# Kernel optimization log

Hardware: AMD Instinct MI355X
Metric: run time of the kernel (lower is better)

## Reference

```python
import jax, jax.numpy as jnp
import numpy as np

N_NODES = 50000
N_EDGES = 800000
HID = 64
NUM_CURR = 15
NUM_PAY = 7
CURR_DIM = 8
PAY_DIM = 4
NUM_NUM = 5
EDGE_REPR = 2 * HID + 2 * CURR_DIM + PAY_DIM + NUM_NUM  # 153


def setup_inputs() -> dict:
    key = jax.random.key(0)
    ks = jax.random.split(key, 24)
    f = lambda k, shape, scale=0.05: jax.random.normal(k, shape, jnp.float32) * scale
    inp = {
        'node_feats': jax.random.normal(ks[0], (N_NODES, 2), jnp.float32),
        'src': jax.random.randint(ks[1], (N_EDGES,), 0, N_NODES, jnp.int32),
        'dst': jax.random.randint(ks[2], (N_EDGES,), 0, N_NODES, jnp.int32),
        'payment_currency': jax.random.randint(ks[3], (N_EDGES,), 0, NUM_CURR, jnp.int32),
        'receiving_currency': jax.random.randint(ks[4], (N_EDGES,), 0, NUM_CURR, jnp.int32),
        'payment_format': jax.random.randint(ks[5], (N_EDGES,), 0, NUM_PAY, jnp.int32),
        'numericals': jax.random.normal(ks[6], (N_EDGES, NUM_NUM), jnp.float32),
        # GCN layer params
        'W0': f(ks[7], (2, HID)), 'b0': f(ks[8], (HID,)),
        'W1': f(ks[9], (HID, HID)), 'b1': f(ks[10], (HID,)),
        'W2': f(ks[11], (HID, HID)), 'b2': f(ks[12], (HID,)),
        # edge embeddings
        'curr_emb': f(ks[13], (NUM_CURR, CURR_DIM), 1.0),
        'pay_emb': f(ks[14], (NUM_PAY, PAY_DIM), 1.0),
        # edge classifier MLP
        'M0': f(ks[15], (EDGE_REPR, HID)), 'bM0': f(ks[16], (HID,)),
        'M1': f(ks[17], (HID, HID)), 'bM1': f(ks[18], (HID,)),
        'M2': f(ks[19], (HID, 2)), 'bM2': f(ks[20], (2,)),
    }
    return inp


def reference(node_feats, src, dst, payment_currency, receiving_currency,
              payment_format, numericals, W0, b0, W1, b1, W2, b2,
              curr_emb, pay_emb, M0, bM0, M1, bM1, M2, bM2):
    # symmetric-ish GCN norm: deg^{-1/2} on source (message) and dest (after sum)
    ones = jnp.ones((src.shape[0],), jnp.float32)
    deg = jax.ops.segment_sum(ones, dst, num_segments=N_NODES)
    norm = jnp.clip(deg, 1.0, None) ** -0.5  # [N]
    norm = norm[:, None]

    def gcn(h, W, b, residual):
        Wh = h @ W + b                         # [N, HID]
        m = Wh[src] * norm[src]                # gather-scale per edge [E, HID]
        agg = jax.ops.segment_sum(m, dst, num_segments=N_NODES)  # scatter-sum
        out = jax.nn.relu(agg * norm)
        return out + h if residual else out    # res_linear is Identity (dims match)

    h = gcn(node_feats, W0, b0, False)
    h = gcn(h, W1, b1, True)
    h = gcn(h, W2, b2, True)
    # dropout is inference no-op

    edge_repr = jnp.concatenate([
        h[src], h[dst],
        curr_emb[payment_currency], curr_emb[receiving_currency],
        pay_emb[payment_format], numericals,
    ], axis=1)  # [E, 153]

    x = jax.nn.relu(edge_repr @ M0 + bM0)
    x = jax.nn.relu(x @ M1 + bM1)
    logits = x @ M2 + bM2  # [E, 2]
    return logits
```

## Files before the change

kernel.cpp:

```cpp
#include <hip/hip_runtime.h>
#include <hip/hip_bf16.h>

#define N_NODES 50000
#define N_EDGES 800000
#define HID 64

__device__ __forceinline__ unsigned short f2bf(float f) {
    union { float f; unsigned int i; } v;
    v.f = f;
    unsigned int b = v.i;
    return (unsigned short)((b + 0x7FFFu + ((b >> 16) & 1u)) >> 16);
}

__device__ __forceinline__ void add_bf16_row(float* x, const unsigned short* row) {
    const uint4* r4 = (const uint4*)row;
#pragma unroll
    for (int q = 0; q < 8; ++q) {
        uint4 v = r4[q];
        union { unsigned int i; float f; } t;
        t.i = v.x << 16;         x[q*8 + 0] += t.f;
        t.i = v.x & 0xFFFF0000u; x[q*8 + 1] += t.f;
        t.i = v.y << 16;         x[q*8 + 2] += t.f;
        t.i = v.y & 0xFFFF0000u; x[q*8 + 3] += t.f;
        t.i = v.z << 16;         x[q*8 + 4] += t.f;
        t.i = v.z & 0xFFFF0000u; x[q*8 + 5] += t.f;
        t.i = v.w << 16;         x[q*8 + 6] += t.f;
        t.i = v.w & 0xFFFF0000u; x[q*8 + 7] += t.f;
    }
}


__global__ void k_deg(const int* __restrict__ dst, int* __restrict__ deg, int n) {
    int e = blockIdx.x * blockDim.x + threadIdx.x;
    if (e < n) atomicAdd(&deg[dst[e]], 1);
}

__global__ void k_off(const int* __restrict__ deg, int* __restrict__ row_ptr,
                      int* __restrict__ cursor, float* __restrict__ norm,
                      int* __restrict__ gcount, int n) {
    int i = blockIdx.x * blockDim.x + threadIdx.x;
    int lane = threadIdx.x & 63;
    int v = (i < n) ? deg[i] : 0;
    int s = v;
#pragma unroll
    for (int off = 1; off < 64; off <<= 1) {
        int t = __shfl_up(s, off);
        if (lane >= off) s += t;
    }
    int total = __shfl(s, 63);
    int base = 0;
    if (lane == 63) base = atomicAdd(gcount, total);
    base = __shfl(base, 63);
    int ex = base + s - v;
    if (i < n) {
        row_ptr[i] = ex;
        cursor[i]  = ex;
        norm[i] = 1.0f / sqrtf(fmaxf((float)v, 1.0f));
    }
}

__global__ void k_scatter(const int* __restrict__ src, const int* __restrict__ dst,
                          int* __restrict__ cursor, int* __restrict__ csr_src, int n) {
    int e = blockIdx.x * blockDim.x + threadIdx.x;
    if (e < n) {
        int d = dst[e];
        int pos = atomicAdd(&cursor[d], 1);
        csr_src[pos] = src[e];
    }
}


__global__ __launch_bounds__(256) void k_l0(const float2* __restrict__ nf,
                                            const float* __restrict__ norm,
                                            const int* __restrict__ row_ptr,
                                            const int* __restrict__ deg,
                                            const int* __restrict__ csr_src,
                                            const float* __restrict__ W0,
                                            const float* __restrict__ b0,
                                            float* __restrict__ h,
                                            float* __restrict__ hn,
                                            float* __restrict__ snorm, int n_nodes) {
    int lane = threadIdx.x & 63, wid = threadIdx.x >> 6;
    int n = blockIdx.x * 4 + wid;
    if (n >= n_nodes) return;
    int r0 = row_ptr[n], dc = deg[n];
    float a0 = 0.f, a1 = 0.f, sn = 0.f;
    for (int i = lane; i < dc; i += 64) {
        int s = csr_src[r0 + i];
        float ns = norm[s];
        float2 v = nf[s];
        a0 += v.x * ns;
        a1 += v.y * ns;
        sn += ns;
    }
#pragma unroll
    for (int off = 32; off; off >>= 1) {
        a0 += __shfl_xor(a0, off);
        a1 += __shfl_xor(a1, off);
        sn += __shfl_xor(sn, off);
    }
    float nn = norm[n];
    float v = (a0 * W0[lane] + a1 * W0[64 + lane] + b0[lane] * sn) * nn;
    v = fmaxf(v, 0.f);
    h[(size_t)n * 64 + lane] = v;
    hn[(size_t)n * 64 + lane] = v * nn;
    if (lane == 0) snorm[n] = sn;
}


__global__ __launch_bounds__(256) void k_agg(const float* __restrict__ hn,
                                             const int* __restrict__ row_ptr,
                                             const int* __restrict__ deg,
                                             const int* __restrict__ csr_src,
                                             float* __restrict__ g, int n_nodes) {
    int lane = threadIdx.x & 63, wid = threadIdx.x >> 6;
    int n = blockIdx.x * 4 + wid;
    if (n >= n_nodes) return;
    int r0 = row_ptr[n], dc = deg[n];
    float acc = 0.f;
    int i = 0;
    for (; i + 4 <= dc; i += 4) {
        int s0 = csr_src[r0 + i + 0];
        int s1 = csr_src[r0 + i + 1];
        int s2 = csr_src[r0 + i + 2];
        int s3 = csr_src[r0 + i + 3];
        float v0 = hn[(size_t)s0 * 64 + lane];
        float v1 = hn[(size_t)s1 * 64 + lane];
        float v2 = hn[(size_t)s2 * 64 + lane];
        float v3 = hn[(size_t)s3 * 64 + lane];
        acc += (v0 + v1) + (v2 + v3);
    }
    for (; i < dc; ++i) acc += hn[(size_t)csr_src[r0 + i] * 64 + lane];
    g[(size_t)n * 64 + lane] = acc;
}


__global__ __launch_bounds__(256) void k_mv(const float* __restrict__ g,
                                            const float* __restrict__ h_in,
                                            const float* __restrict__ W,
                                            const float* __restrict__ b,
                                            const float* __restrict__ norm,
                                            const float* __restrict__ snorm,
                                            float* __restrict__ h_out,
                                            float* __restrict__ hn_out, int n_nodes) {
    int lane = threadIdx.x & 63, wid = threadIdx.x >> 6;
    int n = blockIdx.x * 64 + lane;
    if (n >= n_nodes) return;
    const int j0 = wid * 16;
    float sn = snorm[n];
    float y[16];
    const float* bj = b + j0;
#pragma unroll
    for (int q = 0; q < 16; ++q) y[q] = bj[q] * sn;
    const float4* g4 = (const float4*)(g + (size_t)n * 64);
    const float* Wj = W + j0;
#pragma unroll
    for (int k4 = 0; k4 < 16; ++k4) {
        float4 xv = g4[k4];
        const float* w0 = Wj + (k4 * 4 + 0) * 64;
        const float* w1 = Wj + (k4 * 4 + 1) * 64;
        const float* w2 = Wj + (k4 * 4 + 2) * 64;
        const float* w3 = Wj + (k4 * 4 + 3) * 64;
#pragma unroll
        for (int q = 0; q < 16; ++q) {
            y[q] = fmaf(xv.x, w0[q], y[q]);
            y[q] = fmaf(xv.y, w1[q], y[q]);
            y[q] = fmaf(xv.z, w2[q], y[q]);
            y[q] = fmaf(xv.w, w3[q], y[q]);
        }
    }
    float nn = norm[n];
    const float4* h4 = (const float4*)(h_in + (size_t)n * 64 + j0);
    float4* o4 = (float4*)(h_out + (size_t)n * 64 + j0);
#pragma unroll
    for (int q4 = 0; q4 < 4; ++q4) {
        float4 hv = h4[q4];
        float4 ov;
        ov.x = fmaxf(y[q4*4+0] * nn, 0.f) + hv.x;
        ov.y = fmaxf(y[q4*4+1] * nn, 0.f) + hv.y;
        ov.z = fmaxf(y[q4*4+2] * nn, 0.f) + hv.z;
        ov.w = fmaxf(y[q4*4+3] * nn, 0.f) + hv.w;
        o4[q4] = ov;
    }
    if (hn_out) {
        float4* s4 = (float4*)(hn_out + (size_t)n * 64 + j0);
#pragma unroll
        for (int q4 = 0; q4 < 4; ++q4) {
            float4 ov = o4[q4];
            float4 sv;
            sv.x = ov.x * nn; sv.y = ov.y * nn; sv.z = ov.z * nn; sv.w = ov.w * nn;
            s4[q4] = sv;
        }
    }
}


__global__ __launch_bounds__(512) void k_mv2(const float* __restrict__ h,
                                             const float* __restrict__ M0,
                                             unsigned short* __restrict__ Ab,
                                             unsigned short* __restrict__ Bb,
                                             int n_nodes) {
    int lane = threadIdx.x & 63, wid = threadIdx.x >> 6;
    int n = blockIdx.x * 64 + lane;
    if (n >= n_nodes) return;
    const int tbl = wid >> 2;
    const int j0 = (wid & 3) * 16;
    float y[16];
#pragma unroll
    for (int q = 0; q < 16; ++q) y[q] = 0.f;
    const float4* h4 = (const float4*)(h + (size_t)n * 64);
    const float* Wj = M0 + tbl * 4096 + j0;
#pragma unroll
    for (int k4 = 0; k4 < 16; ++k4) {
        float4 xv = h4[k4];
        const float* w0 = Wj + (k4 * 4 + 0) * 64;
        const float* w1 = Wj + (k4 * 4 + 1) * 64;
        const float* w2 = Wj + (k4 * 4 + 2) * 64;
        const float* w3 = Wj + (k4 * 4 + 3) * 64;
#pragma unroll
        for (int q = 0; q < 16; ++q) {
            y[q] = fmaf(xv.x, w0[q], y[q]);
            y[q] = fmaf(xv.y, w1[q], y[q]);
            y[q] = fmaf(xv.z, w2[q], y[q]);
            y[q] = fmaf(xv.w, w3[q], y[q]);
        }
    }
    unsigned short* Ot = (tbl ? Bb : Ab) + (size_t)n * 64 + j0;
    uint4* o4 = (uint4*)Ot;
#pragma unroll
    for (int q = 0; q < 2; ++q) {
        uint4 ov;
        ov.x = (unsigned int)f2bf(y[q*8+0]) | ((unsigned int)f2bf(y[q*8+1]) << 16);
        ov.y = (unsigned int)f2bf(y[q*8+2]) | ((unsigned int)f2bf(y[q*8+3]) << 16);
        ov.z = (unsigned int)f2bf(y[q*8+4]) | ((unsigned int)f2bf(y[q*8+5]) << 16);
        ov.w = (unsigned int)f2bf(y[q*8+6]) | ((unsigned int)f2bf(y[q*8+7]) << 16);
        o4[q] = ov;
    }
}


__global__ void k_small(const float* __restrict__ curr_emb, const float* __restrict__ pay_emb,
                        const float* __restrict__ M0, float* __restrict__ C1,
                        float* __restrict__ C2, float* __restrict__ P) {
    int tid = threadIdx.x;
    for (int idx = tid; idx < 15 * 64; idx += blockDim.x) {
        int c = idx >> 6, j = idx & 63;
        float s1 = 0.f, s2 = 0.f;
        for (int k = 0; k < 8; ++k) {
            float ce = curr_emb[c * 8 + k];
            s1 += ce * M0[(128 + k) * 64 + j];
            s2 += ce * M0[(136 + k) * 64 + j];
        }
        C1[idx] = s1;
        C2[idx] = s2;
    }
    for (int idx = tid; idx < 7 * 64; idx += blockDim.x) {
        int p = idx >> 6, j = idx & 63;
        float s = 0.f;
        for (int k = 0; k < 4; ++k) s += pay_emb[p * 4 + k] * M0[(144 + k) * 64 + j];
        P[idx] = s;
    }
}

__global__ void k_combo(const float* __restrict__ C1, const float* __restrict__ C2,
                        const float* __restrict__ P, const float* __restrict__ bM0,
                        float* __restrict__ T, int total) {
    int idx = blockIdx.x * blockDim.x + threadIdx.x;
    if (idx < total) {
        int j = idx & 63, c = idx >> 6;
        int p = c % 7, cc = c / 7;
        int c2 = cc % 15, c1 = cc / 15;
        T[idx] = C1[c1 * 64 + j] + C2[c2 * 64 + j] + P[p * 64 + j] + bM0[j];
    }
}


__global__ __launch_bounds__(256, 2) void k_edge(const unsigned short* __restrict__ Ab,
                                                 const unsigned short* __restrict__ Bb,
                                                 const float* __restrict__ T,
                                                 const float* __restrict__ M0,
                                                 const float* __restrict__ M1,
                                                 const float* __restrict__ bM1,
                                                 const float* __restrict__ M2,
                                                 const float* __restrict__ bM2,
                                                 const int* __restrict__ src,
                                                 const int* __restrict__ dst,
                                                 const int* __restrict__ pc,
                                                 const int* __restrict__ rc,
                                                 const int* __restrict__ pf,
                                                 const float* __restrict__ num,
                                                 float* __restrict__ out, int n_edges) {
    int e = blockIdx.x * blockDim.x + threadIdx.x;
    if (e >= n_edges) return;
    int s = src[e], d = dst[e];
    int combo = (pc[e] * 15 + rc[e]) * 7 + pf[e];
    float nk[5];
#pragma unroll
    for (int k = 0; k < 5; ++k) nk[k] = num[(size_t)e * 5 + k];

    float x0[64];
    const float4* t4 = (const float4*)(T + (size_t)combo * 64);
#pragma unroll
    for (int q = 0; q < 16; ++q) {
        float4 v = t4[q];
        x0[q*4+0] = v.x; x0[q*4+1] = v.y; x0[q*4+2] = v.z; x0[q*4+3] = v.w;
    }
    add_bf16_row(x0, Ab + (size_t)s * 64);
    add_bf16_row(x0, Bb + (size_t)d * 64);
#pragma unroll
    for (int k = 0; k < 5; ++k) {
        const float* m4 = M0 + (148 + k) * 64;
        float nkk = nk[k];
#pragma unroll
        for (int q = 0; q < 64; ++q) x0[q] = fmaf(nkk, m4[q], x0[q]);
    }
#pragma unroll
    for (int k = 0; k < 64; ++k) x0[k] = fmaxf(x0[k], 0.f);

    float lg0 = bM2[0], lg1 = bM2[1];
#pragma unroll
    for (int jh = 0; jh < 2; ++jh) {
        float x1[32];
        const float* bb = bM1 + jh * 32;
#pragma unroll
        for (int q = 0; q < 32; ++q) x1[q] = bb[q];
#pragma unroll
        for (int k = 0; k < 64; ++k) {
            float xk = x0[k];
            const float* mr = M1 + k * 64 + jh * 32;
#pragma unroll
            for (int q = 0; q < 32; ++q) x1[q] = fmaf(xk, mr[q], x1[q]);
        }
#pragma unroll
        for (int j = 0; j < 32; ++j) {
            float xv = fmaxf(x1[j], 0.f);
            int jj = jh * 32 + j;
            lg0 = fmaf(xv, M2[jj * 2 + 0], lg0);
            lg1 = fmaf(xv, M2[jj * 2 + 1], lg1);
        }
    }
    ((float2*)out)[e] = make_float2(lg0, lg1);
}


extern "C" void kernel_launch(void* const* d_in, const int* in_sizes, int n_in,
                              void* d_out, int out_size, void* d_ws, size_t ws_size,
                              hipStream_t stream) {
    const float2* node_feats = (const float2*)d_in[0];
    const int*   src  = (const int*)d_in[1];
    const int*   dst  = (const int*)d_in[2];
    const int*   pc   = (const int*)d_in[3];
    const int*   rc   = (const int*)d_in[4];
    const int*   pf   = (const int*)d_in[5];
    const float* num  = (const float*)d_in[6];
    const float* W0   = (const float*)d_in[7];
    const float* b0   = (const float*)d_in[8];
    const float* W1   = (const float*)d_in[9];
    const float* b1   = (const float*)d_in[10];
    const float* W2   = (const float*)d_in[11];
    const float* b2   = (const float*)d_in[12];
    const float* curr_emb = (const float*)d_in[13];
    const float* pay_emb  = (const float*)d_in[14];
    const float* M0   = (const float*)d_in[15];
    const float* bM0  = (const float*)d_in[16];
    const float* M1   = (const float*)d_in[17];
    const float* bM1  = (const float*)d_in[18];
    const float* M2   = (const float*)d_in[19];
    const float* bM2  = (const float*)d_in[20];
    float* out = (float*)d_out;

    char* w = (char*)d_ws;
    auto alloc = [&](size_t bytes) {
        char* p = w;
        w += (bytes + 255) & ~size_t(255);
        return p;
    };
    int*    deg     = (int*)alloc(N_NODES * 4);
    int*    gcount  = (int*)alloc(256);
    float*  norm    = (float*)alloc(N_NODES * 4);
    float*  snorm   = (float*)alloc(N_NODES * 4);
    int*    row_ptr = (int*)alloc((N_NODES + 1) * 4);
    int*    cursor  = (int*)alloc(N_NODES * 4);
    int*    csr_src = (int*)alloc(N_EDGES * 4);
    float*  B1      = (float*)alloc(N_NODES * HID * 4);
    float*  B2      = (float*)alloc(N_NODES * HID * 4);
    float*  B3      = (float*)alloc(N_NODES * HID * 4);
    float*  B4      = (float*)alloc(N_NODES * HID * 4);
    unsigned short* Ab = (unsigned short*)alloc(N_NODES * HID * 2);
    unsigned short* Bb = (unsigned short*)alloc(N_NODES * HID * 2);
    float*  C1      = (float*)alloc(15 * 64 * 4);
    float*  C2      = (float*)alloc(15 * 64 * 4);
    float*  P       = (float*)alloc(7 * 64 * 4);
    float*  T       = (float*)alloc(15 * 15 * 7 * 64 * 4);

    hipMemsetAsync(deg, 0, N_NODES * 4, stream);
    hipMemsetAsync(gcount, 0, 256, stream);
    k_deg<<<(N_EDGES + 255) / 256, 256, 0, stream>>>(dst, deg, N_EDGES);
    k_off<<<(N_NODES + 255) / 256, 256, 0, stream>>>(deg, row_ptr, cursor, norm, gcount, N_NODES);
    k_scatter<<<(N_EDGES + 255) / 256, 256, 0, stream>>>(src, dst, cursor, csr_src, N_EDGES);
    k_l0<<<(N_NODES + 3) / 4, 256, 0, stream>>>(node_feats, norm, row_ptr, deg, csr_src,
                                                W0, b0, B1, B2, snorm, N_NODES);
    k_agg<<<(N_NODES + 3) / 4, 256, 0, stream>>>(B2, row_ptr, deg, csr_src, B3, N_NODES);
    k_mv<<<(N_NODES + 63) / 64, 256, 0, stream>>>(B3, B1, W1, b1, norm, snorm, B4, B2, N_NODES);
    k_agg<<<(N_NODES + 3) / 4, 256, 0, stream>>>(B2, row_ptr, deg, csr_src, B3, N_NODES);
    k_mv<<<(N_NODES + 63) / 64, 256, 0, stream>>>(B3, B4, W2, b2, norm, snorm, B1, nullptr, N_NODES);
    k_small<<<1, 256, 0, stream>>>(curr_emb, pay_emb, M0, C1, C2, P);
    k_combo<<<(15 * 15 * 7 * 64 + 255) / 256, 256, 0, stream>>>(C1, C2, P, bM0, T, 15 * 15 * 7 * 64);
    k_mv2<<<(N_NODES + 63) / 64, 512, 0, stream>>>(B1, M0, Ab, Bb, N_NODES);
    k_edge<<<(N_EDGES + 255) / 256, 256, 0, stream>>>(Ab, Bb, T, M0, M1, bM1, M2, bM2,
                                                      src, dst, pc, rc, pf, num, out, N_EDGES);
}
```

Baseline: 622.0 us.

## Store scaled node features in bf16 and use packed fp32 math in edge MLP

The normalized node features gathered by the aggregation kernel are now stored as bf16 instead of fp32, which halves the bytes read in the gather-heavy aggregation step. Separately, the per-edge MLP is rewritten with two-wide float vectors and elementwise fma/max builtins so the compiler can emit packed fp32 instructions. The cost is lower precision in the aggregated messages, plus some extra conversion work.

```diff
diff --git a/kernel.cpp b/kernel.cpp
--- a/kernel.cpp
+++ b/kernel.cpp
@@ -4,6 +4,8 @@
 #define N_NODES 50000
 #define N_EDGES 800000
 #define HID 64
+
+typedef __attribute__((ext_vector_type(2))) float f32x2;
 
 __device__ __forceinline__ unsigned short f2bf(float f) {
     union { float f; unsigned int i; } v;
@@ -12,21 +14,20 @@
     return (unsigned short)((b + 0x7FFFu + ((b >> 16) & 1u)) >> 16);
 }
 
-__device__ __forceinline__ void add_bf16_row(float* x, const unsigned short* row) {
-    const uint4* r4 = (const uint4*)row;
-#pragma unroll
-    for (int q = 0; q < 8; ++q) {
-        uint4 v = r4[q];
-        union { unsigned int i; float f; } t;
-        t.i = v.x << 16;         x[q*8 + 0] += t.f;
-        t.i = v.x & 0xFFFF0000u; x[q*8 + 1] += t.f;
-        t.i = v.y << 16;         x[q*8 + 2] += t.f;
-        t.i = v.y & 0xFFFF0000u; x[q*8 + 3] += t.f;
-        t.i = v.z << 16;         x[q*8 + 4] += t.f;
-        t.i = v.z & 0xFFFF0000u; x[q*8 + 5] += t.f;
-        t.i = v.w << 16;         x[q*8 + 6] += t.f;
-        t.i = v.w & 0xFFFF0000u; x[q*8 + 7] += t.f;
-    }
+__device__ __forceinline__ float bf2f(unsigned short u) {
+    union { unsigned int i; float f; } t;
+    t.i = ((unsigned int)u) << 16;
+    return t.f;
+}
+
+__device__ __forceinline__ f32x2 bfpair(unsigned int u) {
+    union { unsigned int i; float f; } lo, hi;
+    lo.i = u << 16;
+    hi.i = u & 0xFFFF0000u;
+    f32x2 r;
+    r[0] = lo.f;
+    r[1] = hi.f;
+    return r;
 }
 
 
@@ -78,7 +79,7 @@
                                             const float* __restrict__ W0,
                                             const float* __restrict__ b0,
                                             float* __restrict__ h,
-                                            float* __restrict__ hn,
+                                            unsigned short* __restrict__ hn,
                                             float* __restrict__ snorm, int n_nodes) {
     int lane = threadIdx.x & 63, wid = threadIdx.x >> 6;
     int n = blockIdx.x * 4 + wid;
@@ -103,12 +104,12 @@
     float v = (a0 * W0[lane] + a1 * W0[64 + lane] + b0[lane] * sn) * nn;
     v = fmaxf(v, 0.f);
     h[(size_t)n * 64 + lane] = v;
-    hn[(size_t)n * 64 + lane] = v * nn;
+    hn[(size_t)n * 64 + lane] = f2bf(v * nn);
     if (lane == 0) snorm[n] = sn;
 }
 
 
-__global__ __launch_bounds__(256) void k_agg(const float* __restrict__ hn,
+__global__ __launch_bounds__(256) void k_agg(const unsigned short* __restrict__ hn,
                                              const int* __restrict__ row_ptr,
                                              const int* __restrict__ deg,
                                              const int* __restrict__ csr_src,
@@ -124,13 +125,13 @@
         int s1 = csr_src[r0 + i + 1];
         int s2 = csr_src[r0 + i + 2];
         int s3 = csr_src[r0 + i + 3];
-        float v0 = hn[(size_t)s0 * 64 + lane];
-        float v1 = hn[(size_t)s1 * 64 + lane];
-        float v2 = hn[(size_t)s2 * 64 + lane];
-        float v3 = hn[(size_t)s3 * 64 + lane];
+        float v0 = bf2f(hn[(size_t)s0 * 64 + lane]);
+        float v1 = bf2f(hn[(size_t)s1 * 64 + lane]);
+        float v2 = bf2f(hn[(size_t)s2 * 64 + lane]);
+        float v3 = bf2f(hn[(size_t)s3 * 64 + lane]);
         acc += (v0 + v1) + (v2 + v3);
     }
-    for (; i < dc; ++i) acc += hn[(size_t)csr_src[r0 + i] * 64 + lane];
+    for (; i < dc; ++i) acc += bf2f(hn[(size_t)csr_src[r0 + i] * 64 + lane]);
     g[(size_t)n * 64 + lane] = acc;
 }
 
@@ -142,7 +143,7 @@
                                             const float* __restrict__ norm,
                                             const float* __restrict__ snorm,
                                             float* __restrict__ h_out,
-                                            float* __restrict__ hn_out, int n_nodes) {
+                                            unsigned short* __restrict__ hn_out, int n_nodes) {
     int lane = threadIdx.x & 63, wid = threadIdx.x >> 6;
     int n = blockIdx.x * 64 + lane;
     if (n >= n_nodes) return;
@@ -172,24 +173,28 @@
     float nn = norm[n];
     const float4* h4 = (const float4*)(h_in + (size_t)n * 64 + j0);
     float4* o4 = (float4*)(h_out + (size_t)n * 64 + j0);
+    float ov[16];
 #pragma unroll
     for (int q4 = 0; q4 < 4; ++q4) {
         float4 hv = h4[q4];
-        float4 ov;
-        ov.x = fmaxf(y[q4*4+0] * nn, 0.f) + hv.x;
-        ov.y = fmaxf(y[q4*4+1] * nn, 0.f) + hv.y;
-        ov.z = fmaxf(y[q4*4+2] * nn, 0.f) + hv.z;
-        ov.w = fmaxf(y[q4*4+3] * nn, 0.f) + hv.w;
-        o4[q4] = ov;
+        float4 o;
+        o.x = fmaxf(y[q4*4+0] * nn, 0.f) + hv.x;
+        o.y = fmaxf(y[q4*4+1] * nn, 0.f) + hv.y;
+        o.z = fmaxf(y[q4*4+2] * nn, 0.f) + hv.z;
+        o.w = fmaxf(y[q4*4+3] * nn, 0.f) + hv.w;
+        o4[q4] = o;
+        ov[q4*4+0] = o.x; ov[q4*4+1] = o.y; ov[q4*4+2] = o.z; ov[q4*4+3] = o.w;
     }
     if (hn_out) {
-        float4* s4 = (float4*)(hn_out + (size_t)n * 64 + j0);
-#pragma unroll
-        for (int q4 = 0; q4 < 4; ++q4) {
-            float4 ov = o4[q4];
-            float4 sv;
-            sv.x = ov.x * nn; sv.y = ov.y * nn; sv.z = ov.z * nn; sv.w = ov.w * nn;
-            s4[q4] = sv;
+        uint4* s4 = (uint4*)(hn_out + (size_t)n * 64 + j0);
+#pragma unroll
+        for (int q8 = 0; q8 < 2; ++q8) {
+            uint4 w;
+            w.x = (unsigned int)f2bf(ov[q8*8+0] * nn) | ((unsigned int)f2bf(ov[q8*8+1] * nn) << 16);
+            w.y = (unsigned int)f2bf(ov[q8*8+2] * nn) | ((unsigned int)f2bf(ov[q8*8+3] * nn) << 16);
+            w.z = (unsigned int)f2bf(ov[q8*8+4] * nn) | ((unsigned int)f2bf(ov[q8*8+5] * nn) << 16);
+            w.w = (unsigned int)f2bf(ov[q8*8+6] * nn) | ((unsigned int)f2bf(ov[q8*8+7] * nn) << 16);
+            s4[q8] = w;
         }
     }
 }
@@ -298,45 +303,66 @@
 #pragma unroll
     for (int k = 0; k < 5; ++k) nk[k] = num[(size_t)e * 5 + k];
 
-    float x0[64];
-    const float4* t4 = (const float4*)(T + (size_t)combo * 64);
-#pragma unroll
-    for (int q = 0; q < 16; ++q) {
-        float4 v = t4[q];
-        x0[q*4+0] = v.x; x0[q*4+1] = v.y; x0[q*4+2] = v.z; x0[q*4+3] = v.w;
-    }
-    add_bf16_row(x0, Ab + (size_t)s * 64);
-    add_bf16_row(x0, Bb + (size_t)d * 64);
+    f32x2 x0[32];
+    const f32x2* t2 = (const f32x2*)(T + (size_t)combo * 64);
+#pragma unroll
+    for (int q = 0; q < 32; ++q) x0[q] = t2[q];
+
+    const uint4* ra = (const uint4*)(Ab + (size_t)s * 64);
+#pragma unroll
+    for (int q = 0; q < 8; ++q) {
+        uint4 v = ra[q];
+        x0[q*4+0] += bfpair(v.x);
+        x0[q*4+1] += bfpair(v.y);
+        x0[q*4+2] += bfpair(v.z);
+        x0[q*4+3] += bfpair(v.w);
+    }
+    const uint4* rb = (const uint4*)(Bb + (size_t)d * 64);
+#pragma unroll
+    for (int q = 0; q < 8; ++q) {
+        uint4 v = rb[q];
+        x0[q*4+0] += bfpair(v.x);
+        x0[q*4+1] += bfpair(v.y);
+        x0[q*4+2] += bfpair(v.z);
+        x0[q*4+3] += bfpair(v.w);
+    }
 #pragma unroll
     for (int k = 0; k < 5; ++k) {
-        const float* m4 = M0 + (148 + k) * 64;
-        float nkk = nk[k];
-#pragma unroll
-        for (int q = 0; q < 64; ++q) x0[q] = fmaf(nkk, m4[q], x0[q]);
-    }
-#pragma unroll
-    for (int k = 0; k < 64; ++k) x0[k] = fmaxf(x0[k], 0.f);
+        const f32x2* mp = (const f32x2*)(M0 + (148 + k) * 64);
+        f32x2 nv;
+        nv[0] = nk[k]; nv[1] = nk[k];
+#pragma unroll
+        for (int q = 0; q < 32; ++q) x0[q] = __builtin_elementwise_fma(nv, mp[q], x0[q]);
+    }
+    f32x2 zero2;
+    zero2[0] = 0.f; zero2[1] = 0.f;
+#pragma unroll
+    for (int q = 0; q < 32; ++q) x0[q] = __builtin_elementwise_max(x0[q], zero2);
 
     float lg0 = bM2[0], lg1 = bM2[1];
 #pragma unroll
     for (int jh = 0; jh < 2; ++jh) {
-        float x1[32];
-        const float* bb = bM1 + jh * 32;
-#pragma unroll
-        for (int q = 0; q < 32; ++q) x1[q] = bb[q];
+        f32x2 x1[16];
+        const f32x2* bb = (const f32x2*)(bM1 + jh * 32);
+#pragma unroll
+        for (int q = 0; q < 16; ++q) x1[q] = bb[q];
 #pragma unroll
         for (int k = 0; k < 64; ++k) {
-            float xk = x0[k];
-            const float* mr = M1 + k * 64 + jh * 32;
-#pragma unroll
-            for (int q = 0; q < 32; ++q) x1[q] = fmaf(xk, mr[q], x1[q]);
-        }
-#pragma unroll
-        for (int j = 0; j < 32; ++j) {
-            float xv = fmaxf(x1[j], 0.f);
-            int jj = jh * 32 + j;
-            lg0 = fmaf(xv, M2[jj * 2 + 0], lg0);
-            lg1 = fmaf(xv, M2[jj * 2 + 1], lg1);
+            float xk = x0[k >> 1][k & 1];
+            f32x2 xv;
+            xv[0] = xk; xv[1] = xk;
+            const f32x2* mr = (const f32x2*)(M1 + k * 64 + jh * 32);
+#pragma unroll
+            for (int q = 0; q < 16; ++q) x1[q] = __builtin_elementwise_fma(xv, mr[q], x1[q]);
+        }
+#pragma unroll
+        for (int q = 0; q < 16; ++q) {
+            f32x2 xv = __builtin_elementwise_max(x1[q], zero2);
+            int j = jh * 32 + q * 2;
+            lg0 = fmaf(xv[0], M2[j * 2 + 0], lg0);
+            lg1 = fmaf(xv[0], M2[j * 2 + 1], lg1);
+            lg0 = fmaf(xv[1], M2[j * 2 + 2], lg0);
+            lg1 = fmaf(xv[1], M2[j * 2 + 3], lg1);
         }
     }
     ((float2*)out)[e] = make_float2(lg0, lg1);
@@ -383,7 +409,7 @@
     int*    cursor  = (int*)alloc(N_NODES * 4);
     int*    csr_src = (int*)alloc(N_EDGES * 4);
     float*  B1      = (float*)alloc(N_NODES * HID * 4);
-    float*  B2      = (float*)alloc(N_NODES * HID * 4);
+    unsigned short* B2 = (unsigned short*)alloc(N_NODES * HID * 2);
     float*  B3      = (float*)alloc(N_NODES * HID * 4);
     float*  B4      = (float*)alloc(N_NODES * HID * 4);
     unsigned short* Ab = (unsigned short*)alloc(N_NODES * HID * 2);
```

Measured after the change: 602.3 us. 3.2% less time.
